# Kernel tuning notes

Hardware: AMD Instinct MI355X
Metric: run time of the kernel (lower is better)

## Reference

```python
import jax, jax.numpy as jnp
import numpy as np

EPS = 1e-5
D, C, T, H = 512, 256, 2, 2  # d_model, d_ctx, tokens, heads
HD = D // H                   # head dim


def _ln(x, g, b):
    m = x.mean(-1, keepdims=True)
    v = ((x - m) ** 2).mean(-1, keepdims=True)
    return (x - m) / jnp.sqrt(v + EPS) * g + b


def setup_inputs() -> dict:
    key = jax.random.key(0)
    ks = jax.random.split(key, 16)
    B, L = 8, 4096
    w = lambda k, s: (jax.random.normal(k, s, jnp.float32) * 0.02)
    Hc, H2 = 512, 1024  # ctx-head hidden = max(D,C); mix hidden = 2*D
    return {
        "x": jax.random.normal(ks[0], (B, L, D), jnp.float32),
        "context": jax.random.normal(ks[1], (B, C), jnp.float32),
        "pad_valid_mask": jax.random.bernoulli(ks[2], 0.9, (B, L)),
        "film_ln_g": jnp.ones(D), "film_ln_b": jnp.zeros(D),
        "film_w": w(ks[3], (2 * D, C)), "film_b": jnp.zeros(2 * D),
        "concat_w": w(ks[4], (D, D + C)), "concat_b": jnp.zeros(D),
        "concat_ln_g": jnp.ones(D), "concat_ln_b": jnp.zeros(D),
        "ctx_w1": w(ks[5], (Hc, C)), "ctx_b1": jnp.zeros(Hc),
        "ctx_w2": w(ks[6], (T * D, Hc)), "ctx_b2": jnp.zeros(T * D),
        "q_ln_g": jnp.ones(D), "q_ln_b": jnp.zeros(D),
        "in_proj_w": w(ks[7], (3 * D, D)), "in_proj_b": jnp.zeros(3 * D),
        "out_proj_w": w(ks[8], (D, D)), "out_proj_b": jnp.zeros(D),
        "mix_w1": w(ks[9], (H2, 4 * D)), "mix_b1": jnp.zeros(H2),
        "mix_w2": w(ks[10], (D, H2)), "mix_b2": jnp.zeros(D),
        "out_ln_g": jnp.ones(D), "out_ln_b": jnp.zeros(D),
        "gate_w": w(ks[11], (D, C)), "gate_b": jnp.zeros(D),
    }


def reference(x, context, pad_valid_mask,
              film_ln_g, film_ln_b, film_w, film_b,
              concat_w, concat_b, concat_ln_g, concat_ln_b,
              ctx_w1, ctx_b1, ctx_w2, ctx_b2,
              q_ln_g, q_ln_b, in_proj_w, in_proj_b, out_proj_w, out_proj_b,
              mix_w1, mix_b1, mix_w2, mix_b2,
              out_ln_g, out_ln_b, gate_w, gate_b):
    B, L, _ = x.shape
    film_gain, alpha_max = 1.0, 1.0
    # 1) HyperFiLM: base = (1 + gain*gamma) * LN(x) + gain*beta
    gb = context @ film_w.T + film_b                      # [B, 2D]
    gamma, beta = gb[:, :D], gb[:, D:]
    base = (1.0 + film_gain * gamma)[:, None, :] * _ln(x, film_ln_g, film_ln_b) \
           + (film_gain * beta)[:, None, :]
    # 2) Concat path
    ctx_exp = jnp.broadcast_to(context[:, None, :], (B, L, C))
    z = jnp.concatenate([x, ctx_exp], axis=-1)            # [B, L, D+C]
    upd_c = _ln(jax.nn.relu(z @ concat_w.T + concat_b), concat_ln_g, concat_ln_b)
    # 3) Cross-attn path: context -> T tokens
    h = jax.nn.gelu(context @ ctx_w1.T + ctx_b1, approximate=False)
    ctx_tok = (h @ ctx_w2.T + ctx_b2).reshape(B, T, D)
    x_q = _ln(x, q_ln_g, q_ln_b)
    wq, wk, wv = in_proj_w[:D], in_proj_w[D:2 * D], in_proj_w[2 * D:]
    bq, bk, bv = in_proj_b[:D], in_proj_b[D:2 * D], in_proj_b[2 * D:]
    q = (x_q @ wq.T + bq).reshape(B, L, H, HD)
    k = (ctx_tok @ wk.T + bk).reshape(B, T, H, HD)
    v = (ctx_tok @ wv.T + bv).reshape(B, T, H, HD)
    scores = jnp.einsum('blhd,bthd->bhlt', q, k) / jnp.sqrt(jnp.float32(HD))
    attn = jax.nn.softmax(scores, axis=-1)
    a = jnp.einsum('bhlt,bthd->blhd', attn, v).reshape(B, L, D)
    attn_out = a @ out_proj_w.T + out_proj_b
    mix_in = jnp.concatenate([x, attn_out, x - attn_out, x * attn_out], axis=-1)
    upd_a = jax.nn.relu(mix_in @ mix_w1.T + mix_b1) @ mix_w2.T + mix_b2
    # 4) Combine with sigmoid gate, alpha, pad mask
    gate = jax.nn.sigmoid(context @ gate_w.T + gate_b) * alpha_max  # [B, D]
    gate = gate[:, None, :] * pad_valid_mask[:, :, None].astype(x.dtype)
    out = _ln(base + gate * (upd_c + upd_a), out_ln_g, out_ln_b)
    return out
```

## Files before the change

### kernel.cpp

```cpp
#include <hip/hip_runtime.h>
#include <hip/hip_bf16.h>


#define N_TOK 32768
#define HALF_ROWS 16384

typedef unsigned short u16;
typedef __attribute__((ext_vector_type(8))) __bf16 bf16x8;
typedef __attribute__((ext_vector_type(4))) float f32x4;

__device__ __forceinline__ float bf2f(unsigned int h) { return __uint_as_float(h << 16); }
__device__ __forceinline__ u16 f2bf(float f) {
    unsigned int u = __float_as_uint(f);
    u += 0x7FFFu + ((u >> 16) & 1u);
    return (u16)(u >> 16);
}
__device__ __forceinline__ void load8(const u16* p, float* v) {
    uint4 u = *(const uint4*)p;
    v[0] = bf2f(u.x & 0xffffu); v[1] = bf2f(u.x >> 16);
    v[2] = bf2f(u.y & 0xffffu); v[3] = bf2f(u.y >> 16);
    v[4] = bf2f(u.z & 0xffffu); v[5] = bf2f(u.z >> 16);
    v[6] = bf2f(u.w & 0xffffu); v[7] = bf2f(u.w >> 16);
}
__device__ __forceinline__ uint4 pack8(const float* v) {
    uint4 u;
    u.x = (unsigned)f2bf(v[0]) | ((unsigned)f2bf(v[1]) << 16);
    u.y = (unsigned)f2bf(v[2]) | ((unsigned)f2bf(v[3]) << 16);
    u.z = (unsigned)f2bf(v[4]) | ((unsigned)f2bf(v[5]) << 16);
    u.w = (unsigned)f2bf(v[6]) | ((unsigned)f2bf(v[7]) << 16);
    return u;
}
__device__ __forceinline__ void async16(const u16* g, u16* lds) {
    __builtin_amdgcn_global_load_lds(
        (const __attribute__((address_space(1))) unsigned int*)g,
        (__attribute__((address_space(3))) unsigned int*)lds, 16, 0, 0);
}

#define FENCE() asm volatile("" ::: "memory")
#define BARRIER() do { FENCE(); __builtin_amdgcn_s_barrier(); FENCE(); } while (0)
#define WAITV(n) asm volatile("s_waitcnt vmcnt(" #n ")" ::: "memory")
#define LGKM0()  asm volatile("s_waitcnt lgkmcnt(0)" ::: "memory")

__global__ void prep_kernel(const float* __restrict__ in_proj_w,
                            const float* __restrict__ in_proj_b,
                            const float* __restrict__ qb,
                            const float* __restrict__ concat_w,
                            const float* __restrict__ mix_w1,
                            const float* __restrict__ mix_w2,
                            const float* __restrict__ context,
                            float* __restrict__ bqp,
                            u16* __restrict__ cwbf, u16* __restrict__ m1bf,
                            u16* __restrict__ m2bf, u16* __restrict__ ctxbf) {
    const int bid = blockIdx.x;
    const int tid = threadIdx.x;
    if (bid < 128) {
        const int wave = tid >> 6, lane = tid & 63;
        const int j = bid * 4 + wave;
        const int i = lane * 8;
        float4 w0 = *(const float4*)(in_proj_w + (size_t)j * 512 + i);
        float4 w1 = *(const float4*)(in_proj_w + (size_t)j * 512 + i + 4);
        float4 b0 = *(const float4*)(qb + i);
        float4 b1 = *(const float4*)(qb + i + 4);
        float p1 = w0.x*b0.x + w0.y*b0.y + w0.z*b0.z + w0.w*b0.w
                 + w1.x*b1.x + w1.y*b1.y + w1.z*b1.z + w1.w*b1.w;
        for (int m = 1; m < 64; m <<= 1) p1 += __shfl_xor(p1, m, 64);
        if (lane == 0) bqp[j] = in_proj_b[j] + p1;
    } else if (bid < 320) {
        int i = (bid - 128) * 256 + tid;
        const float* s = concat_w + (size_t)i * 8;
        float4 a = *(const float4*)s;
        float4 b = *(const float4*)(s + 4);
        float v[8] = {a.x, a.y, a.z, a.w, b.x, b.y, b.z, b.w};
        *(uint4*)(cwbf + (size_t)i * 8) = pack8(v);
    } else if (bid < 576) {
        int i = (bid - 320) * 256 + tid;
        const float* s = mix_w2 + (size_t)i * 8;
        float4 a = *(const float4*)s;
        float4 b = *(const float4*)(s + 4);
        float v[8] = {a.x, a.y, a.z, a.w, b.x, b.y, b.z, b.w};
        *(uint4*)(m2bf + (size_t)i * 8) = pack8(v);
    } else if (bid < 1344) {
        int idx = (bid - 576) * 256 + tid;
        int n = idx / 192;
        int k = (idx - n * 192) * 8;
        const float* base = mix_w1 + (size_t)n * 2048;
        float v[8];
        if (k < 512) {
            #pragma unroll
            for (int e = 0; e < 8; e++) v[e] = base[k + e] + base[1024 + k + e];
        } else if (k < 1024) {
            #pragma unroll
            for (int e = 0; e < 8; e++) v[e] = base[k + e] - base[512 + k + e];
        } else {
            #pragma unroll
            for (int e = 0; e < 8; e++) v[e] = base[512 + k + e];
        }
        *(uint4*)(m1bf + (size_t)n * 1536 + k) = pack8(v);
    } else {
        for (int i = tid; i < 2048; i += 256)
            ctxbf[i] = f2bf(context[i]);
    }
}

__global__ void ctx_stage_a(const float* __restrict__ context,
                            const float* __restrict__ film_w, const float* __restrict__ film_b,
                            const float* __restrict__ gate_w, const float* __restrict__ gate_b,
                            const float* __restrict__ ctx_w1, const float* __restrict__ ctx_b1,
                            float* __restrict__ gb1, float* __restrict__ betab,
                            float* __restrict__ gateb, float* __restrict__ hbuf) {
    const int wave = threadIdx.x >> 6, lane = threadIdx.x & 63;
    const int widx = blockIdx.x * 4 + wave;
    const int b   = widx >> 11;
    const int j2  = widx & 2047;
    const int cat = j2 >> 9;
    const int j   = j2 & 511;
    const float* wrow;
    if      (cat == 0) wrow = film_w + (size_t)j * 256;
    else if (cat == 1) wrow = film_w + (size_t)(512 + j) * 256;
    else if (cat == 2) wrow = gate_w + (size_t)j * 256;
    else               wrow = ctx_w1 + (size_t)j * 256;
    float4 wv = *(const float4*)(wrow + lane * 4);
    float4 cv = *(const float4*)(context + b * 256 + lane * 4);
    float s = wv.x * cv.x + wv.y * cv.y + wv.z * cv.z + wv.w * cv.w;
    for (int m = 1; m < 64; m <<= 1) s += __shfl_xor(s, m, 64);
    if (lane == 0) {
        if      (cat == 0) gb1[b * 512 + j]   = 1.0f + s + film_b[j];
        else if (cat == 1) betab[b * 512 + j] = s + film_b[512 + j];
        else if (cat == 2) gateb[b * 512 + j] = 1.f / (1.f + expf(-(s + gate_b[j])));
        else {
            float hv = s + ctx_b1[j];
            hbuf[b * 512 + j] = 0.5f * hv * (1.0f + erff(hv * 0.70710678118654752f));
        }
    }
}

__global__ void ctx_stage_b(const float* __restrict__ hbuf,
                            const float* __restrict__ ctx_w2, const float* __restrict__ ctx_b2,
                            float* __restrict__ tokbuf) {
    const int wave = threadIdx.x >> 6, lane = threadIdx.x & 63;
    const int widx = blockIdx.x * 4 + wave;
    const int b = widx >> 10;
    const int j = widx & 1023;
    const float* wrow = ctx_w2 + (size_t)j * 512 + lane * 8;
    const float* hr   = hbuf + b * 512 + lane * 8;
    float4 w0 = *(const float4*)wrow, w1 = *(const float4*)(wrow + 4);
    float4 h0 = *(const float4*)hr,   h1 = *(const float4*)(hr + 4);
    float s = w0.x*h0.x + w0.y*h0.y + w0.z*h0.z + w0.w*h0.w
            + w1.x*h1.x + w1.y*h1.y + w1.z*h1.z + w1.w*h1.w;
    for (int m = 1; m < 64; m <<= 1) s += __shfl_xor(s, m, 64);
    if (lane == 0) tokbuf[b * 1024 + j] = s + ctx_b2[j];
}

__global__ void ctx_stage_c(const float* __restrict__ tokbuf,
                            const float* __restrict__ in_proj_w, const float* __restrict__ in_proj_b,
                            float* __restrict__ kbuf, float* __restrict__ vbuf) {
    const int wave = threadIdx.x >> 6, lane = threadIdx.x & 63;
    const int widx = blockIdx.x * 4 + wave;
    const int b  = widx >> 11;
    const int r  = widx & 2047;
    const int t  = r >> 10;
    const int kv = (r >> 9) & 1;
    const int j  = r & 511;
    const float* wrow = in_proj_w + (size_t)(512 + kv * 512 + j) * 512 + lane * 8;
    const float* tk   = tokbuf + (b * 2 + t) * 512 + lane * 8;
    float4 w0 = *(const float4*)wrow, w1 = *(const float4*)(wrow + 4);
    float4 t0 = *(const float4*)tk,   t1 = *(const float4*)(tk + 4);
    float s = w0.x*t0.x + w0.y*t0.y + w0.z*t0.z + w0.w*t0.w
            + w1.x*t1.x + w1.y*t1.y + w1.z*t1.z + w1.w*t1.w;
    for (int m = 1; m < 64; m <<= 1) s += __shfl_xor(s, m, 64);
    if (lane == 0) {
        float v = s + in_proj_b[512 + kv * 512 + j];
        if (kv == 0) kbuf[(b * 2 + t) * 512 + j] = v;
        else         vbuf[(b * 2 + t) * 512 + j] = v;
    }
}

__global__ void ctx_stage_d(const float* __restrict__ in_proj_w,
                            const float* __restrict__ out_proj_w,
                            const float* __restrict__ qg, const float* __restrict__ bqp,
                            const float* __restrict__ kbuf, const float* __restrict__ vbuf,
                            float* __restrict__ ubuf, float* __restrict__ vobuf,
                            float* __restrict__ subuf, float* __restrict__ c0buf) {
    const int tid = threadIdx.x;
    __shared__ float sh[256];
    __shared__ float red[256];
    if (blockIdx.x < 32) {
        const int bid = blockIdx.x;
        const int b = bid >> 2, idx = bid & 3;
        const int t = idx >> 1, h = idx & 1;
        sh[tid] = kbuf[(b * 2 + t) * 512 + h * 256 + tid];
        __syncthreads();
        float a0 = 0.f, a1 = 0.f;
        #pragma unroll 4
        for (int dd = 0; dd < 256; dd++) {
            const float kv = sh[dd];
            const float* wr = in_proj_w + (size_t)(h * 256 + dd) * 512;
            a0 += kv * wr[tid];
            a1 += kv * wr[tid + 256];
        }
        float u0 = a0 * qg[tid], u1 = a1 * qg[tid + 256];
        ubuf[bid * 512 + tid]       = u0;
        ubuf[bid * 512 + tid + 256] = u1;
        red[tid] = u0 + u1;
        __syncthreads();
        for (int s = 128; s > 0; s >>= 1) { if (tid < s) red[tid] += red[tid + s]; __syncthreads(); }
        if (tid == 0) subuf[bid] = red[0];
        __syncthreads();
        red[tid] = bqp[h * 256 + tid] * sh[tid];
        __syncthreads();
        for (int s = 128; s > 0; s >>= 1) { if (tid < s) red[tid] += red[tid + s]; __syncthreads(); }
        if (tid == 0) c0buf[bid] = red[0];
    } else {
        const int bid = blockIdx.x - 32;
        const int b = bid >> 2, idx = bid & 3;
        const int t = idx >> 1, h = idx & 1;
        sh[tid] = vbuf[(b * 2 + t) * 512 + h * 256 + tid];
        __syncthreads();
        const float* w0 = out_proj_w + (size_t)tid * 512 + h * 256;
        const float* w1 = out_proj_w + (size_t)(tid + 256) * 512 + h * 256;
        float acc0 = 0.f, acc1 = 0.f;
        #pragma unroll 2
        for (int dd = 0; dd < 256; dd += 4) {
            float4 x0 = *(const float4*)(w0 + dd);
            float4 x1 = *(const float4*)(w1 + dd);
            acc0 += x0.x*sh[dd] + x0.y*sh[dd+1] + x0.z*sh[dd+2] + x0.w*sh[dd+3];
            acc1 += x1.x*sh[dd] + x1.y*sh[dd+1] + x1.z*sh[dd+2] + x1.w*sh[dd+3];
        }
        vobuf[bid * 512 + tid]       = acc0;
        vobuf[bid * 512 + tid + 256] = acc1;
    }
}

__global__ void statsattn_kernel(const float* __restrict__ x, float* __restrict__ stats,
                                 u16* __restrict__ mixA, u16* __restrict__ pbufH,
                                 const float* __restrict__ ubuf, const float* __restrict__ subuf,
                                 const float* __restrict__ c0buf, const float* __restrict__ vobuf,
                                 const float* __restrict__ ob, const int rowbase) {
    const int wave = threadIdx.x >> 6, lane = threadIdx.x & 63;
    const size_t lr = (size_t)blockIdx.x * 8 + wave * 2;
    const size_t gr = lr + rowbase;
    const int b = (int)(gr >> 12);
    float v[2][8], s[2] = {0.f, 0.f}, ss[2] = {0.f, 0.f};
    #pragma unroll
    for (int r = 0; r < 2; r++) {
        const float* xr = x + (gr + r) * 512 + lane * 8;
        float4 a = *(const float4*)xr;
        float4 c = *(const float4*)(xr + 4);
        v[r][0]=a.x; v[r][1]=a.y; v[r][2]=a.z; v[r][3]=a.w;
        v[r][4]=c.x; v[r][5]=c.y; v[r][6]=c.z; v[r][7]=c.w;
        #pragma unroll
        for (int e = 0; e < 8; e++) { s[r] += v[r][e]; ss[r] += v[r][e] * v[r][e]; }
    }
    float u[4][8];
    #pragma unroll
    for (int idx = 0; idx < 4; idx++) {
        const float* up = ubuf + (b * 4 + idx) * 512 + lane * 8;
        float4 u0 = *(const float4*)up, u1 = *(const float4*)(up + 4);
        u[idx][0]=u0.x; u[idx][1]=u0.y; u[idx][2]=u0.z; u[idx][3]=u0.w;
        u[idx][4]=u1.x; u[idx][5]=u1.y; u[idx][6]=u1.z; u[idx][7]=u1.w;
    }
    float sd[2][4];
    #pragma unroll
    for (int r = 0; r < 2; r++)
        #pragma unroll
        for (int idx = 0; idx < 4; idx++) {
            float acc = 0.f;
            #pragma unroll
            for (int e = 0; e < 8; e++) acc += v[r][e] * u[idx][e];
            sd[r][idx] = acc;
        }
    for (int m = 1; m < 64; m <<= 1) {
        #pragma unroll
        for (int r = 0; r < 2; r++) {
            s[r] += __shfl_xor(s[r], m, 64); ss[r] += __shfl_xor(ss[r], m, 64);
            #pragma unroll
            for (int idx = 0; idx < 4; idx++) sd[r][idx] += __shfl_xor(sd[r][idx], m, 64);
        }
    }
    float vo[4][8];
    #pragma unroll
    for (int idx = 0; idx < 4; idx++) {
        const float* vp = vobuf + (b * 4 + idx) * 512 + lane * 8;
        float4 v0 = *(const float4*)vp, v1 = *(const float4*)(vp + 4);
        vo[idx][0]=v0.x; vo[idx][1]=v0.y; vo[idx][2]=v0.z; vo[idx][3]=v0.w;
        vo[idx][4]=v1.x; vo[idx][5]=v1.y; vo[idx][6]=v1.z; vo[idx][7]=v1.w;
    }
    float obp[8];
    {
        const float* op = ob + lane * 8;
        float4 o0 = *(const float4*)op, o1 = *(const float4*)(op + 4);
        obp[0]=o0.x; obp[1]=o0.y; obp[2]=o0.z; obp[3]=o0.w;
        obp[4]=o1.x; obp[5]=o1.y; obp[6]=o1.z; obp[7]=o1.w;
    }
    #pragma unroll
    for (int r = 0; r < 2; r++) {
        const float mean = s[r] * (1.f / 512.f);
        const float rstd = rsqrtf(ss[r] * (1.f / 512.f) - mean * mean + 1e-5f);
        if (lane == 0) { stats[(gr + r) * 2] = mean; stats[(gr + r) * 2 + 1] = rstd; }
        float sc[4];
        #pragma unroll
        for (int idx = 0; idx < 4; idx++)
            sc[idx] = (rstd * (sd[r][idx] - mean * subuf[b * 4 + idx]) + c0buf[b * 4 + idx]) * (1.f / 16.f);
        float p[4];
        #pragma unroll
        for (int h = 0; h < 2; h++) {
            float s0 = sc[h], s1 = sc[2 + h];
            float mx = fmaxf(s0, s1);
            float e0 = expf(s0 - mx), e1 = expf(s1 - mx);
            float inv = 1.f / (e0 + e1);
            p[h] = e0 * inv; p[2 + h] = e1 * inv;
        }
        float o[8], pr[8];
        #pragma unroll
        for (int e = 0; e < 8; e++) {
            o[e] = p[0]*vo[0][e] + p[1]*vo[1][e] + p[2]*vo[2][e] + p[3]*vo[3][e] + obp[e];
            pr[e] = v[r][e] * o[e];
        }
        *(uint4*)(mixA + (gr + r) * 1024 + lane * 8)       = pack8(v[r]);
        *(uint4*)(mixA + (gr + r) * 1024 + 512 + lane * 8) = pack8(o);
        *(uint4*)(pbufH + (lr + r) * 512 + lane * 8)       = pack8(pr);
    }
}

template<int AMODE, bool RELU>
__launch_bounds__(256)
__global__ void mfma_gemm(const u16* __restrict__ A0, const u16* __restrict__ A1,
                          const u16* __restrict__ Wb, const float* __restrict__ bias,
                          u16* __restrict__ out, const int K, const int lda, const int ldo) {
    __shared__ __align__(16) u16 S[16384];
    u16* As = S;
    u16* Bs = S + 8192;
    const int tid = threadIdx.x;
    const int w = tid >> 6, l = tid & 63;
    const int wm = w >> 1, wn = w & 1;
    const size_t m0 = (size_t)blockIdx.x * 128;
    const int n0 = blockIdx.y * 128;
    const int rb = w * 8 + (l >> 3);
    const int kswz = ((l & 7) ^ (l >> 3)) * 8;
    const int bidx = (int)(m0 >> 12);
    const int quad = l >> 4, lc = l & 15;

    f32x4 acc[4][4];
    #pragma unroll
    for (int i = 0; i < 4; i++)
        #pragma unroll
        for (int j = 0; j < 4; j++) acc[i][j] = (f32x4){0.f, 0.f, 0.f, 0.f};

    for (int k0 = 0; k0 < K; k0 += 64) {
        __syncthreads();
        if constexpr (AMODE == 0) {
            #pragma unroll
            for (int r = 0; r < 4; r++)
                async16(A0 + (m0 + r * 32 + rb) * (size_t)lda + k0 + kswz, &As[r * 2048 + w * 512]);
        } else {
            if (k0 < 512) {
                #pragma unroll
                for (int r = 0; r < 4; r++)
                    async16(A0 + (m0 + r * 32 + rb) * (size_t)lda + k0 + kswz, &As[r * 2048 + w * 512]);
            } else {
                #pragma unroll
                for (int r = 0; r < 4; r++)
                    async16(A1 + bidx * 256 + (k0 - 512) + kswz, &As[r * 2048 + w * 512]);
            }
        }
        #pragma unroll
        for (int r = 0; r < 4; r++)
            async16(Wb + (size_t)(n0 + r * 32 + rb) * K + k0 + kswz, &Bs[r * 2048 + w * 512]);
        __syncthreads();
        #pragma unroll
        for (int kk = 0; kk < 2; kk++) {
            bf16x8 af[4], bff[4];
            #pragma unroll
            for (int t = 0; t < 4; t++) {
                const int ch = ((kk << 2) | quad) ^ (lc & 7);
                af[t]  = *(const bf16x8*)&As[(wm * 64 + t * 16 + lc) * 64 + ch * 8];
                bff[t] = *(const bf16x8*)&Bs[(wn * 64 + t * 16 + lc) * 64 + ch * 8];
            }
            #pragma unroll
            for (int i = 0; i < 4; i++)
                #pragma unroll
                for (int j = 0; j < 4; j++)
                    acc[i][j] = __builtin_amdgcn_mfma_f32_16x16x32_bf16(af[i], bff[j], acc[i][j], 0, 0, 0);
        }
    }

    float bv[4];
    #pragma unroll
    for (int j = 0; j < 4; j++) bv[j] = bias[n0 + wn * 64 + j * 16 + lc];
    const int erow = tid >> 2;
    const int ecb  = (tid & 3) * 32;
    __syncthreads();
    #pragma unroll
    for (int p = 0; p < 2; p++) {
        if (p) __syncthreads();
        if (wm == p) {
            #pragma unroll
            for (int i = 0; i < 4; i++)
                #pragma unroll
                for (int j = 0; j < 4; j++)
                    #pragma unroll
                    for (int reg = 0; reg < 4; reg++) {
                        float vv = acc[i][j][reg] + bv[j];
                        if (RELU) vv = fmaxf(vv, 0.f);
                        S[(i * 16 + quad * 4 + reg) * 136 + wn * 64 + j * 16 + lc] = f2bf(vv);
                    }
        }
        __syncthreads();
        #pragma unroll
        for (int q = 0; q < 4; q++)
            *(uint4*)(out + (m0 + p * 64 + erow) * (size_t)ldo + n0 + ecb + q * 8)
                = *(const uint4*)&S[erow * 136 + ecb + q * 8];
    }
}

__launch_bounds__(512, 2)
__global__ void mix1_gemm8(const u16* __restrict__ A0, const u16* __restrict__ A1,
                           const u16* __restrict__ Wb, const float* __restrict__ bias,
                           u16* __restrict__ out) {
    extern __shared__ __align__(16) u16 S[];
    u16* As = S;
    u16* Bs = S + 32768;
    const int tid = threadIdx.x;
    const int l = tid & 63;
    const int w = tid >> 6;
    const int wm = w >> 2, wn = w & 3;
    const int quad = l >> 4, lc = l & 15;
    const size_t m0 = (size_t)blockIdx.x * 256;
    const int n0 = blockIdx.y * 256;

    const int r0 = tid >> 3;
    const int r1 = (tid + 512) >> 3;
    const int c0s = ((tid & 7) ^ (r0 & 7)) * 8;
    const int c1s = ((tid & 7) ^ (r1 & 7)) * 8;

    auto stA = [&](int kt, int h, int buf) {
        u16* dst = As + (buf * 2 + h) * 8192;
        if (kt < 16) {
            async16(A0 + (m0 + h * 128 + r0) * 1024 + kt * 64 + c0s, dst + tid * 8);
            async16(A0 + (m0 + h * 128 + r1) * 1024 + kt * 64 + c1s, dst + (tid + 512) * 8);
        } else {
            async16(A1 + (m0 + h * 128 + r0) * 512 + (kt - 16) * 64 + c0s, dst + tid * 8);
            async16(A1 + (m0 + h * 128 + r1) * 512 + (kt - 16) * 64 + c1s, dst + (tid + 512) * 8);
        }
    };
    auto stB = [&](int kt, int h, int buf) {
        u16* dst = Bs + (buf * 2 + h) * 8192;
        async16(Wb + (size_t)(n0 + h * 128 + r0) * 1536 + kt * 64 + c0s, dst + tid * 8);
        async16(Wb + (size_t)(n0 + h * 128 + r1) * 1536 + kt * 64 + c1s, dst + (tid + 512) * 8);
    };

    bf16x8 a_[4][2], b_[2][2][2];
    f32x4 acc[8][4];
    #pragma unroll
    for (int i = 0; i < 8; i++)
        #pragma unroll
        for (int j = 0; j < 4; j++) acc[i][j] = (f32x4){0.f, 0.f, 0.f, 0.f};

    auto rdA = [&](int buf, int qi) {
        const u16* Ab = As + (buf * 2 + wm) * 8192;
        #pragma unroll
        for (int ii = 0; ii < 4; ii++) {
            const int r = (qi * 4 + ii) * 16 + lc;
            #pragma unroll
            for (int kk = 0; kk < 2; kk++) {
                const int cs = (kk * 4 + quad) ^ (r & 7);
                a_[ii][kk] = *(const bf16x8*)&Ab[r * 64 + cs * 8];
            }
        }
    };
    auto rdB = [&](int buf, int qj) {
        #pragma unroll
        for (int jj = 0; jj < 2; jj++) {
            const int nr = wn * 64 + (qj * 2 + jj) * 16 + lc;
            const int hb = nr >> 7, r = nr & 127;
            const u16* Bb = Bs + (buf * 2 + hb) * 8192;
            #pragma unroll
            for (int kk = 0; kk < 2; kk++) {
                const int cs = (kk * 4 + quad) ^ (r & 7);
                b_[qj][jj][kk] = *(const bf16x8*)&Bb[r * 64 + cs * 8];
            }
        }
    };
    auto mfma16 = [&](int qi, int qj) {
        __builtin_amdgcn_s_setprio(1);
        #pragma unroll
        for (int ii = 0; ii < 4; ii++)
            #pragma unroll
            for (int jj = 0; jj < 2; jj++)
                #pragma unroll
                for (int kk = 0; kk < 2; kk++)
                    acc[qi * 4 + ii][qj * 2 + jj] = __builtin_amdgcn_mfma_f32_16x16x32_bf16(
                        a_[ii][kk], b_[qj][jj][kk], acc[qi * 4 + ii][qj * 2 + jj], 0, 0, 0);
        __builtin_amdgcn_s_setprio(0);
    };

    stA(0, 0, 0); stA(0, 1, 0); stB(0, 0, 0); stB(0, 1, 0);
    stA(1, 0, 1);
    WAITV(2); BARRIER();

    for (int it = 0; it < 12; it++) {
        const int tb = 2 * it + 1;
        const bool more = (it < 11);
        rdA(0, 0); rdB(0, 0);
        stA(tb, 1, 1);
        BARRIER(); mfma16(0, 0);
        rdB(0, 1);
        stB(tb, 0, 1);
        BARRIER(); mfma16(0, 1);
        rdA(0, 1);
        stB(tb, 1, 1);
        BARRIER(); mfma16(1, 1);
        BARRIER();
        if (more) { stA(tb + 1, 0, 0); WAITV(2); }
        else      { WAITV(0); }
        BARRIER(); mfma16(1, 0);
        rdA(1, 0); rdB(1, 0);
        if (more) stA(tb + 1, 1, 0);
        BARRIER(); mfma16(0, 0);
        rdB(1, 1);
        if (more) stB(tb + 1, 0, 0);
        BARRIER(); mfma16(0, 1);
        rdA(1, 1);
        if (more) stB(tb + 1, 1, 0);
        BARRIER(); mfma16(1, 1);
        BARRIER();
        if (more) { stA(tb + 2, 0, 1); WAITV(2); }
        BARRIER(); mfma16(1, 0);
    }

    BARRIER();
    float bv[4];
    #pragma unroll
    for (int j = 0; j < 4; j++) bv[j] = bias[n0 + wn * 64 + j * 16 + lc];
    #pragma unroll
    for (int p = 0; p < 2; p++) {
        if (p) BARRIER();
        if (wm == p) {
            #pragma unroll
            for (int i = 0; i < 8; i++)
                #pragma unroll
                for (int j = 0; j < 4; j++)
                    #pragma unroll
                    for (int reg = 0; reg < 4; reg++) {
                        float vv = fmaxf(acc[i][j][reg] + bv[j], 0.f);
                        S[(i * 16 + quad * 4 + reg) * 264 + wn * 64 + j * 16 + lc] = f2bf(vv);
                    }
        }
        LGKM0(); BARRIER();
        #pragma unroll
        for (int kq = 0; kq < 8; kq++) {
            const int cix = tid + kq * 512;
            const int row = cix >> 5, ch = cix & 31;
            *(uint4*)(out + (m0 + p * 128 + row) * 1024 + n0 + ch * 8)
                = *(const uint4*)&S[row * 264 + ch * 8];
        }
    }
}

__global__ void final_kernel(const u16* __restrict__ mixA, const float* __restrict__ stats,
                             const u16* __restrict__ bufc,
                             const float* __restrict__ cg, const float* __restrict__ cb,
                             const float* __restrict__ gb1, const float* __restrict__ betab,
                             const float* __restrict__ gateb, const int* __restrict__ mask,
                             const float* __restrict__ fg, const float* __restrict__ fb,
                             const float* __restrict__ og, const float* __restrict__ ob,
                             float* __restrict__ out) {
    const int wave = threadIdx.x >> 6, lane = threadIdx.x & 63;
    const size_t row = (size_t)blockIdx.x * 4 + wave;
    const int b = (int)(row >> 12);
    const int c0 = lane * 8;
    float xv[8], uc[8], ua[8];
    load8(mixA + row * 1024 + c0, xv);
    load8(mixA + row * 1024 + 512 + c0, ua);
    load8(bufc + row * 512 + c0, uc);
    float sc = 0.f, ssc = 0.f;
    #pragma unroll
    for (int e = 0; e < 8; e++) { sc += uc[e]; ssc += uc[e] * uc[e]; }
    for (int m = 1; m < 64; m <<= 1) { sc += __shfl_xor(sc, m, 64); ssc += __shfl_xor(ssc, m, 64); }
    const float mc = sc * (1.f / 512.f);
    const float rc = rsqrtf(ssc * (1.f / 512.f) - mc * mc + 1e-5f);
    const float mean = stats[row * 2], rstd = stats[row * 2 + 1];
    const float mf = (mask[row] != 0) ? 1.f : 0.f;
    float y[8];
    float s = 0.f, ss = 0.f;
    #pragma unroll
    for (int e = 0; e < 8; e++) {
        int c = c0 + e;
        float ucn = (uc[e] - mc) * rc * cg[c] + cb[c];
        float xh = (xv[e] - mean) * rstd;
        float base = gb1[b * 512 + c] * (xh * fg[c] + fb[c]) + betab[b * 512 + c];
        float yv = base + gateb[b * 512 + c] * mf * (ucn + ua[e]);
        y[e] = yv; s += yv; ss += yv * yv;
    }
    for (int m = 1; m < 64; m <<= 1) { s += __shfl_xor(s, m, 64); ss += __shfl_xor(ss, m, 64); }
    float mean2 = s * (1.f / 512.f);
    float rstd2 = rsqrtf(ss * (1.f / 512.f) - mean2 * mean2 + 1e-5f);
    float o[8];
    #pragma unroll
    for (int e = 0; e < 8; e++) {
        int c = c0 + e;
        o[e] = (y[e] - mean2) * rstd2 * og[c] + ob[c];
    }
    *(float4*)(out + row * 512 + c0)     = make_float4(o[0], o[1], o[2], o[3]);
    *(float4*)(out + row * 512 + c0 + 4) = make_float4(o[4], o[5], o[6], o[7]);
}

extern "C" void kernel_launch(void* const* d_in, const int* in_sizes, int n_in,
                              void* d_out, int out_size, void* d_ws, size_t ws_size,
                              hipStream_t stream) {
    const float* x          = (const float*)d_in[0];
    const float* context    = (const float*)d_in[1];
    const int*   mask       = (const int*)d_in[2];
    const float* film_ln_g  = (const float*)d_in[3];
    const float* film_ln_b  = (const float*)d_in[4];
    const float* film_w     = (const float*)d_in[5];
    const float* film_b     = (const float*)d_in[6];
    const float* concat_w   = (const float*)d_in[7];
    const float* concat_b   = (const float*)d_in[8];
    const float* concat_ln_g= (const float*)d_in[9];
    const float* concat_ln_b= (const float*)d_in[10];
    const float* ctx_w1     = (const float*)d_in[11];
    const float* ctx_b1     = (const float*)d_in[12];
    const float* ctx_w2     = (const float*)d_in[13];
    const float* ctx_b2     = (const float*)d_in[14];
    const float* q_ln_g     = (const float*)d_in[15];
    const float* q_ln_b     = (const float*)d_in[16];
    const float* in_proj_w  = (const float*)d_in[17];
    const float* in_proj_b  = (const float*)d_in[18];
    const float* out_proj_w = (const float*)d_in[19];
    const float* out_proj_b = (const float*)d_in[20];
    const float* mix_w1     = (const float*)d_in[21];
    const float* mix_b1     = (const float*)d_in[22];
    const float* mix_w2     = (const float*)d_in[23];
    const float* mix_b2     = (const float*)d_in[24];
    const float* out_ln_g   = (const float*)d_in[25];
    const float* out_ln_b   = (const float*)d_in[26];
    const float* gate_w     = (const float*)d_in[27];
    const float* gate_b     = (const float*)d_in[28];
    float* out = (float*)d_out;

    float* gb1    = (float*)d_ws;
    float* betab  = gb1 + 4096;
    float* gateb  = betab + 4096;
    float* kbuf   = gateb + 4096;
    float* vbuf   = kbuf + 8192;
    float* bqp    = vbuf + 8192;
    float* hbuf   = bqp + 512;
    float* tokbuf = hbuf + 4096;
    float* ubuf   = tokbuf + 8192;
    float* vobuf  = ubuf + 16384;
    float* subuf  = vobuf + 16384;
    float* c0buf  = subuf + 32;
    float* stats  = c0buf + 32;
    u16* ctxbf = (u16*)(stats + 65536);
    u16* cwbf  = ctxbf + 2048;
    u16* m1bf  = cwbf + 393216;
    u16* m2bf  = m1bf + 1572864;
    u16* mixA  = m2bf + 524288;
    u16* bufc  = mixA + (size_t)N_TOK * 1024;
    u16* pbufH = bufc + (size_t)N_TOK * 512;
    u16* bufhH = pbufH + (size_t)HALF_ROWS * 512;

    static bool attr_set = false;
    if (!attr_set) {
        hipFuncSetAttribute((const void*)mix1_gemm8,
                            hipFuncAttributeMaxDynamicSharedMemorySize, 131072);
        attr_set = true;
    }

    prep_kernel<<<1345, 256, 0, stream>>>(in_proj_w, in_proj_b, q_ln_b,
                                          concat_w, mix_w1, mix_w2, context,
                                          bqp, cwbf, m1bf, m2bf, ctxbf);
    ctx_stage_a<<<4096, 256, 0, stream>>>(context, film_w, film_b, gate_w, gate_b,
                                          ctx_w1, ctx_b1, gb1, betab, gateb, hbuf);
    ctx_stage_b<<<2048, 256, 0, stream>>>(hbuf, ctx_w2, ctx_b2, tokbuf);
    ctx_stage_c<<<4096, 256, 0, stream>>>(tokbuf, in_proj_w, in_proj_b, kbuf, vbuf);
    ctx_stage_d<<<64, 256, 0, stream>>>(in_proj_w, out_proj_w, q_ln_g, bqp,
                                        kbuf, vbuf, ubuf, vobuf, subuf, c0buf);

    for (int h = 0; h < 2; h++) {
        const int rowbase = h * HALF_ROWS;
        statsattn_kernel<<<HALF_ROWS / 8, 256, 0, stream>>>(
            x, stats, mixA, pbufH, ubuf, subuf, c0buf, vobuf, out_proj_b, rowbase);
        mix1_gemm8<<<dim3(64, 4), 512, 131072, stream>>>(
            mixA + (size_t)rowbase * 1024, pbufH, m1bf, mix_b1, bufhH);
        mfma_gemm<0, false><<<dim3(128, 4), 256, 0, stream>>>(
            bufhH, nullptr, m2bf, mix_b2,
            mixA + (size_t)rowbase * 1024 + 512, 1024, 1024, 1024);
    }

    mfma_gemm<1, true><<<dim3(256, 4), 256, 0, stream>>>(
        mixA, ctxbf, cwbf, concat_b, bufc, 768, 1024, 512);

    final_kernel<<<N_TOK / 4, 256, 0, stream>>>(mixA, stats, bufc,
                                                concat_ln_g, concat_ln_b,
                                                gb1, betab, gateb, mask,
                                                film_ln_g, film_ln_b,
                                                out_ln_g, out_ln_b, out);
    (void)in_sizes; (void)n_in; (void)out_size; (void)ws_size;
}
```

Measured before the change: 460.6 us.

## Generalize 256x256 pipelined GEMM and use it for mix2 and concat GEMMs

Templates the large 512-thread, double-buffered 256x256-tile mix1 GEMM over A-source mode and K depth, and drops the simpler 128x128 single-buffered GEMM. The mix2 and concat GEMMs now run on this kernel. mix2 runs once over all rows instead of per half, with the hidden buffer enlarged to full size and reused for the concat output. The aim is more data reuse and better latency hiding in the two smaller GEMMs, at the cost of a larger workspace footprint and fewer blocks per launch.

```diff
diff --git a/kernel.cpp b/kernel.cpp
--- a/kernel.cpp
+++ b/kernel.cpp
@@ -322,101 +322,13 @@
     }
 }
 
-template<int AMODE, bool RELU>
-__launch_bounds__(256)
-__global__ void mfma_gemm(const u16* __restrict__ A0, const u16* __restrict__ A1,
+template<int AMODE, int NT, bool RELU>
+__launch_bounds__(512, 2)
+__global__ void mix_gemm8(const u16* __restrict__ A0, const u16* __restrict__ A1,
                           const u16* __restrict__ Wb, const float* __restrict__ bias,
-                          u16* __restrict__ out, const int K, const int lda, const int ldo) {
-    __shared__ __align__(16) u16 S[16384];
-    u16* As = S;
-    u16* Bs = S + 8192;
-    const int tid = threadIdx.x;
-    const int w = tid >> 6, l = tid & 63;
-    const int wm = w >> 1, wn = w & 1;
-    const size_t m0 = (size_t)blockIdx.x * 128;
-    const int n0 = blockIdx.y * 128;
-    const int rb = w * 8 + (l >> 3);
-    const int kswz = ((l & 7) ^ (l >> 3)) * 8;
-    const int bidx = (int)(m0 >> 12);
-    const int quad = l >> 4, lc = l & 15;
-
-    f32x4 acc[4][4];
-    #pragma unroll
-    for (int i = 0; i < 4; i++)
-        #pragma unroll
-        for (int j = 0; j < 4; j++) acc[i][j] = (f32x4){0.f, 0.f, 0.f, 0.f};
-
-    for (int k0 = 0; k0 < K; k0 += 64) {
-        __syncthreads();
-        if constexpr (AMODE == 0) {
-            #pragma unroll
-            for (int r = 0; r < 4; r++)
-                async16(A0 + (m0 + r * 32 + rb) * (size_t)lda + k0 + kswz, &As[r * 2048 + w * 512]);
-        } else {
-            if (k0 < 512) {
-                #pragma unroll
-                for (int r = 0; r < 4; r++)
-                    async16(A0 + (m0 + r * 32 + rb) * (size_t)lda + k0 + kswz, &As[r * 2048 + w * 512]);
-            } else {
-                #pragma unroll
-                for (int r = 0; r < 4; r++)
-                    async16(A1 + bidx * 256 + (k0 - 512) + kswz, &As[r * 2048 + w * 512]);
-            }
-        }
-        #pragma unroll
-        for (int r = 0; r < 4; r++)
-            async16(Wb + (size_t)(n0 + r * 32 + rb) * K + k0 + kswz, &Bs[r * 2048 + w * 512]);
-        __syncthreads();
-        #pragma unroll
-        for (int kk = 0; kk < 2; kk++) {
-            bf16x8 af[4], bff[4];
-            #pragma unroll
-            for (int t = 0; t < 4; t++) {
-                const int ch = ((kk << 2) | quad) ^ (lc & 7);
-                af[t]  = *(const bf16x8*)&As[(wm * 64 + t * 16 + lc) * 64 + ch * 8];
-                bff[t] = *(const bf16x8*)&Bs[(wn * 64 + t * 16 + lc) * 64 + ch * 8];
-            }
-            #pragma unroll
-            for (int i = 0; i < 4; i++)
-                #pragma unroll
-                for (int j = 0; j < 4; j++)
-                    acc[i][j] = __builtin_amdgcn_mfma_f32_16x16x32_bf16(af[i], bff[j], acc[i][j], 0, 0, 0);
-        }
-    }
-
-    float bv[4];
-    #pragma unroll
-    for (int j = 0; j < 4; j++) bv[j] = bias[n0 + wn * 64 + j * 16 + lc];
-    const int erow = tid >> 2;
-    const int ecb  = (tid & 3) * 32;
-    __syncthreads();
-    #pragma unroll
-    for (int p = 0; p < 2; p++) {
-        if (p) __syncthreads();
-        if (wm == p) {
-            #pragma unroll
-            for (int i = 0; i < 4; i++)
-                #pragma unroll
-                for (int j = 0; j < 4; j++)
-                    #pragma unroll
-                    for (int reg = 0; reg < 4; reg++) {
-                        float vv = acc[i][j][reg] + bv[j];
-                        if (RELU) vv = fmaxf(vv, 0.f);
-                        S[(i * 16 + quad * 4 + reg) * 136 + wn * 64 + j * 16 + lc] = f2bf(vv);
-                    }
-        }
-        __syncthreads();
-        #pragma unroll
-        for (int q = 0; q < 4; q++)
-            *(uint4*)(out + (m0 + p * 64 + erow) * (size_t)ldo + n0 + ecb + q * 8)
-                = *(const uint4*)&S[erow * 136 + ecb + q * 8];
-    }
-}
-
-__launch_bounds__(512, 2)
-__global__ void mix1_gemm8(const u16* __restrict__ A0, const u16* __restrict__ A1,
-                           const u16* __restrict__ Wb, const float* __restrict__ bias,
-                           u16* __restrict__ out) {
+                          u16* __restrict__ out, const int ldo) {
+    constexpr int BLD = NT * 64;
+    constexpr int NIT = NT / 2;
     extern __shared__ __align__(16) u16 S[];
     u16* As = S;
     u16* Bs = S + 32768;
@@ -427,6 +339,7 @@
     const int quad = l >> 4, lc = l & 15;
     const size_t m0 = (size_t)blockIdx.x * 256;
     const int n0 = blockIdx.y * 256;
+    const int bidx = (int)(m0 >> 12);
 
     const int r0 = tid >> 3;
     const int r1 = (tid + 512) >> 3;
@@ -435,18 +348,31 @@
 
     auto stA = [&](int kt, int h, int buf) {
         u16* dst = As + (buf * 2 + h) * 8192;
-        if (kt < 16) {
+        if constexpr (AMODE == 0) {
             async16(A0 + (m0 + h * 128 + r0) * 1024 + kt * 64 + c0s, dst + tid * 8);
             async16(A0 + (m0 + h * 128 + r1) * 1024 + kt * 64 + c1s, dst + (tid + 512) * 8);
+        } else if constexpr (AMODE == 1) {
+            if (kt < 8) {
+                async16(A0 + (m0 + h * 128 + r0) * 1024 + kt * 64 + c0s, dst + tid * 8);
+                async16(A0 + (m0 + h * 128 + r1) * 1024 + kt * 64 + c1s, dst + (tid + 512) * 8);
+            } else {
+                async16(A1 + bidx * 256 + (kt - 8) * 64 + c0s, dst + tid * 8);
+                async16(A1 + bidx * 256 + (kt - 8) * 64 + c1s, dst + (tid + 512) * 8);
+            }
         } else {
-            async16(A1 + (m0 + h * 128 + r0) * 512 + (kt - 16) * 64 + c0s, dst + tid * 8);
-            async16(A1 + (m0 + h * 128 + r1) * 512 + (kt - 16) * 64 + c1s, dst + (tid + 512) * 8);
+            if (kt < 16) {
+                async16(A0 + (m0 + h * 128 + r0) * 1024 + kt * 64 + c0s, dst + tid * 8);
+                async16(A0 + (m0 + h * 128 + r1) * 1024 + kt * 64 + c1s, dst + (tid + 512) * 8);
+            } else {
+                async16(A1 + (m0 + h * 128 + r0) * 512 + (kt - 16) * 64 + c0s, dst + tid * 8);
+                async16(A1 + (m0 + h * 128 + r1) * 512 + (kt - 16) * 64 + c1s, dst + (tid + 512) * 8);
+            }
         }
     };
     auto stB = [&](int kt, int h, int buf) {
         u16* dst = Bs + (buf * 2 + h) * 8192;
-        async16(Wb + (size_t)(n0 + h * 128 + r0) * 1536 + kt * 64 + c0s, dst + tid * 8);
-        async16(Wb + (size_t)(n0 + h * 128 + r1) * 1536 + kt * 64 + c1s, dst + (tid + 512) * 8);
+        async16(Wb + (size_t)(n0 + h * 128 + r0) * BLD + kt * 64 + c0s, dst + tid * 8);
+        async16(Wb + (size_t)(n0 + h * 128 + r1) * BLD + kt * 64 + c1s, dst + (tid + 512) * 8);
     };
 
     bf16x8 a_[4][2], b_[2][2][2];
@@ -498,9 +424,9 @@
     stA(1, 0, 1);
     WAITV(2); BARRIER();
 
-    for (int it = 0; it < 12; it++) {
+    for (int it = 0; it < NIT; it++) {
         const int tb = 2 * it + 1;
-        const bool more = (it < 11);
+        const bool more = (it < NIT - 1);
         rdA(0, 0); rdB(0, 0);
         stA(tb, 1, 1);
         BARRIER(); mfma16(0, 0);
@@ -542,7 +468,8 @@
                 for (int j = 0; j < 4; j++)
                     #pragma unroll
                     for (int reg = 0; reg < 4; reg++) {
-                        float vv = fmaxf(acc[i][j][reg] + bv[j], 0.f);
+                        float vv = acc[i][j][reg] + bv[j];
+                        if (RELU) vv = fmaxf(vv, 0.f);
                         S[(i * 16 + quad * 4 + reg) * 264 + wn * 64 + j * 16 + lc] = f2bf(vv);
                     }
         }
@@ -551,7 +478,7 @@
         for (int kq = 0; kq < 8; kq++) {
             const int cix = tid + kq * 512;
             const int row = cix >> 5, ch = cix & 31;
-            *(uint4*)(out + (m0 + p * 128 + row) * 1024 + n0 + ch * 8)
+            *(uint4*)(out + (m0 + p * 128 + row) * (size_t)ldo + n0 + ch * 8)
                 = *(const uint4*)&S[row * 264 + ch * 8];
         }
     }
@@ -657,13 +584,17 @@
     u16* m1bf  = cwbf + 393216;
     u16* m2bf  = m1bf + 1572864;
     u16* mixA  = m2bf + 524288;
-    u16* bufc  = mixA + (size_t)N_TOK * 1024;
-    u16* pbufH = bufc + (size_t)N_TOK * 512;
-    u16* bufhH = pbufH + (size_t)HALF_ROWS * 512;
+    u16* bufh  = mixA + (size_t)N_TOK * 1024;
+    u16* bufc  = bufh;
+    u16* pbufH = bufh + (size_t)N_TOK * 1024;
 
     static bool attr_set = false;
     if (!attr_set) {
-        hipFuncSetAttribute((const void*)mix1_gemm8,
+        hipFuncSetAttribute(reinterpret_cast<const void*>(&mix_gemm8<2, 24, true>),
+                            hipFuncAttributeMaxDynamicSharedMemorySize, 131072);
+        hipFuncSetAttribute(reinterpret_cast<const void*>(&mix_gemm8<0, 16, false>),
+                            hipFuncAttributeMaxDynamicSharedMemorySize, 131072);
+        hipFuncSetAttribute(reinterpret_cast<const void*>(&mix_gemm8<1, 12, true>),
                             hipFuncAttributeMaxDynamicSharedMemorySize, 131072);
         attr_set = true;
     }
@@ -682,15 +613,15 @@
         const int rowbase = h * HALF_ROWS;
         statsattn_kernel<<<HALF_ROWS / 8, 256, 0, stream>>>(
             x, stats, mixA, pbufH, ubuf, subuf, c0buf, vobuf, out_proj_b, rowbase);
-        mix1_gemm8<<<dim3(64, 4), 512, 131072, stream>>>(
-            mixA + (size_t)rowbase * 1024, pbufH, m1bf, mix_b1, bufhH);
-        mfma_gemm<0, false><<<dim3(128, 4), 256, 0, stream>>>(
-            bufhH, nullptr, m2bf, mix_b2,
-            mixA + (size_t)rowbase * 1024 + 512, 1024, 1024, 1024);
-    }
-
-    mfma_gemm<1, true><<<dim3(256, 4), 256, 0, stream>>>(
-        mixA, ctxbf, cwbf, concat_b, bufc, 768, 1024, 512);
+        mix_gemm8<2, 24, true><<<dim3(64, 4), 512, 131072, stream>>>(
+            mixA + (size_t)rowbase * 1024, pbufH, m1bf, mix_b1,
+            bufh + (size_t)rowbase * 1024, 1024);
+    }
+    mix_gemm8<0, 16, false><<<dim3(128, 2), 512, 131072, stream>>>(
+        bufh, nullptr, m2bf, mix_b2, mixA + 512, 1024);
+
+    mix_gemm8<1, 12, true><<<dim3(128, 2), 512, 131072, stream>>>(
+        mixA, ctxbf, cwbf, concat_b, bufc, 512);
 
     final_kernel<<<N_TOK / 4, 256, 0, stream>>>(mixA, stats, bufc,
                                                 concat_ln_g, concat_ln_b,
```

After: 424.0 us. -8.0%, faster.
